# Kernel tuning notes

Hardware: AMD Instinct MI355X
Metric: run time of the kernel (lower is better)

## Reference

```python
import jax, jax.numpy as jnp
import numpy as np

N = 100000
E = 1600000
IN_C, HID_C, OUT_C = 64, 64, 40

def setup_inputs() -> dict:
    key = jax.random.key(0)
    ks = jax.random.split(key, 12)
    x = jax.random.normal(ks[0], (N, IN_C), dtype=jnp.float32)
    edge_index = jax.random.randint(ks[1], (2, E), 0, N, dtype=jnp.int32)
    def glorot(k, fan_in, fan_out):
        lim = float(np.sqrt(6.0 / (fan_in + fan_out)))
        return jax.random.uniform(k, (fan_in, fan_out), jnp.float32, -lim, lim)
    return {
        "x": x,
        "edge_index": edge_index,
        "W0_0": glorot(ks[2], IN_C, HID_C), "W1_0": glorot(ks[3], IN_C, HID_C), "b_0": jnp.zeros((HID_C,), jnp.float32),
        "W0_1": glorot(ks[4], HID_C, HID_C), "W1_1": glorot(ks[5], HID_C, HID_C), "b_1": jnp.zeros((HID_C,), jnp.float32),
        "W0_2": glorot(ks[6], HID_C, OUT_C), "W1_2": glorot(ks[7], HID_C, OUT_C), "b_2": jnp.zeros((OUT_C,), jnp.float32),
    }

def _cheb_norm(edge_index, num_nodes, dtype):
    # PyG ChebConv.__norm__ with normalization=None, edge_weight=None -> ones.
    # L = D - A; lambda_max = 2 * max(L weights); scaled: 2L/lambda_max - I.
    src, dst = edge_index[0], edge_index[1]
    w = jnp.ones((edge_index.shape[1],), dtype)
    deg = jax.ops.segment_sum(w, src, num_segments=num_nodes)
    lam = 2.0 * jnp.maximum(jnp.max(deg), jnp.max(-w))
    scale = 2.0 / lam
    norm_edge = -w * scale            # off-diagonal entries
    norm_loop = deg * scale - 1.0     # diagonal entries (self-loop mask subtracts 1)
    return norm_edge, norm_loop

def _spmm(x, src, dst, norm_edge, norm_loop, num_nodes):
    # y[i] = sum_{e: src->i} norm_e * x[src_e] + norm_loop[i] * x[i]
    msg = norm_edge[:, None] * x[src]
    return jax.ops.segment_sum(msg, dst, num_segments=num_nodes) + norm_loop[:, None] * x

def reference(x, edge_index, W0_0, W1_0, b_0, W0_1, W1_1, b_1, W0_2, W1_2, b_2):
    num_nodes = x.shape[0]
    src, dst = edge_index[0], edge_index[1]
    norm_edge, norm_loop = _cheb_norm(edge_index, num_nodes, x.dtype)

    def cheb(h, W0, W1, b):
        # K=2: out = T0(L) h W0 + T1(L) h W1 + b, T0 = I, T1 = scaled L
        Tx1 = _spmm(h, src, dst, norm_edge, norm_loop, num_nodes)
        return h @ W0 + Tx1 @ W1 + b

    h = jax.nn.relu(cheb(x, W0_0, W1_0, b_0))   # dropout is identity in eval mode
    h = jax.nn.relu(cheb(h, W0_1, W1_1, b_1))
    h = cheb(h, W0_2, W1_2, b_2)
    return jax.nn.log_softmax(h, axis=-1)
```

## Files before the change

kernel.cpp:

```cpp
#include <hip/hip_runtime.h>
#include <math.h>

#define N_NODES 100000
#define N_EDGES 1600000
#define OUTC 40
#define PAIRS40 20

#define NC 32
#define CHUNK (N_EDGES / NC)

#define RANGE_H 32768
#define NR_H 4
#define NPAD_H (NR_H * RANGE_H)

#define RANGE_F 16384
#define NR_F 7

#define FILLB (NC * NR_F)
#define NB32 (N_NODES / 32)
#define GEMB ((NB32 + 3) / 4)

#define SCAN_BLOCK 1024
#define SCAN_NBLK ((N_NODES + SCAN_BLOCK - 1) / SCAN_BLOCK)

typedef float vf2 __attribute__((ext_vector_type(2)));
typedef __fp16 f16x2 __attribute__((ext_vector_type(2)));

__device__ inline unsigned pack_bf16x2(float lo, float hi) {
    unsigned a = __float_as_uint(lo), b = __float_as_uint(hi);
    a = (a + 0x7fffu + ((a >> 16) & 1u)) >> 16;
    b = (b + 0x7fffu + ((b >> 16) & 1u)) & 0xffff0000u;
    return a | b;
}
__device__ inline float bf_lo(unsigned u) { return __uint_as_float(u << 16); }
__device__ inline float bf_hi(unsigned u) { return __uint_as_float(u & 0xffff0000u); }

__device__ inline unsigned pk16(float a, float b) {
    f16x2 h = __builtin_amdgcn_cvt_pkrtz(a, b);
    return __builtin_bit_cast(unsigned, h);
}
__device__ inline f16x2 uph(unsigned u) { return __builtin_bit_cast(f16x2, u); }

__device__ inline float fdot2(f16x2 a, f16x2 b, float c) {
#if __has_builtin(__builtin_amdgcn_fdot2)
    return __builtin_amdgcn_fdot2(a, b, c, false);
#else
    float d;
    asm volatile("v_dot2_f32_f16 %0, %1, %2, %3" : "=v"(d) : "v"(a), "v"(b), "v"(c));
    return d;
#endif
}

#define DOT2_KP4(hq, w0_, w1_, w2_, w3_, p)                                  \
    {                                                                        \
        f16x2 h0 = uph((hq).x), h1 = uph((hq).y), h2 = uph((hq).z), h3 = uph((hq).w); \
        a0x[p] = fdot2(h0, uph((w0_).x), a0x[p]);                            \
        a0y[p] = fdot2(h0, uph((w0_).y), a0y[p]);                            \
        a1x[p] = fdot2(h0, uph((w0_).z), a1x[p]);                            \
        a1y[p] = fdot2(h0, uph((w0_).w), a1y[p]);                            \
        a0x[p] = fdot2(h1, uph((w1_).x), a0x[p]);                            \
        a0y[p] = fdot2(h1, uph((w1_).y), a0y[p]);                            \
        a1x[p] = fdot2(h1, uph((w1_).z), a1x[p]);                            \
        a1y[p] = fdot2(h1, uph((w1_).w), a1y[p]);                            \
        a0x[p] = fdot2(h2, uph((w2_).x), a0x[p]);                            \
        a0y[p] = fdot2(h2, uph((w2_).y), a0y[p]);                            \
        a1x[p] = fdot2(h2, uph((w2_).z), a1x[p]);                            \
        a1y[p] = fdot2(h2, uph((w2_).w), a1y[p]);                            \
        a0x[p] = fdot2(h3, uph((w3_).x), a0x[p]);                            \
        a0y[p] = fdot2(h3, uph((w3_).y), a0y[p]);                            \
        a1x[p] = fdot2(h3, uph((w3_).z), a1x[p]);                            \
        a1y[p] = fdot2(h3, uph((w3_).w), a1y[p]);                            \
    }

__global__ __launch_bounds__(1024) void k_hist(const int* __restrict__ src,
                                               const int* __restrict__ dst,
                                               unsigned short* __restrict__ Hs,
                                               unsigned short* __restrict__ Hd) {
    __shared__ unsigned h32[RANGE_H / 2];
    int c = blockIdx.x, r = blockIdx.y;
    const int* a = blockIdx.z ? dst : src;
    unsigned short* H = blockIdx.z ? Hd : Hs;
    for (int k = threadIdx.x; k < RANGE_H / 2; k += 1024) h32[k] = 0;
    __syncthreads();
    int r0 = r * RANGE_H;
    int e0 = c * CHUNK, e1 = e0 + CHUNK;
    for (int e = e0 + threadIdx.x; e < e1; e += 1024) {
        unsigned d = (unsigned)(a[e] - r0);
        if (d < RANGE_H) atomicAdd(&h32[d >> 1], 1u << ((d & 1) * 16));
    }
    __syncthreads();
    for (int k = threadIdx.x; k < RANGE_H; k += 1024)
        H[c * NPAD_H + r0 + k] = (unsigned short)((h32[k >> 1] >> ((k & 1) * 16)) & 0xffffu);
}

__global__ __launch_bounds__(SCAN_BLOCK) void k_scan1(const unsigned short* __restrict__ Hs,
                                                      const unsigned short* __restrict__ Hd,
                                                      int* __restrict__ rowptr,
                                                      int* __restrict__ blocksum,
                                                      int* __restrict__ deg_src,
                                                      int* __restrict__ maxdeg) {
    __shared__ int buf[2][SCAN_BLOCK];
    int t = threadIdx.x;
    int i = blockIdx.x * SCAN_BLOCK + t;
    int vs = 0, vd = 0;
    if (i < N_NODES) {
        #pragma unroll
        for (int c = 0; c < NC; c++) { vs += Hs[c * NPAD_H + i]; vd += Hd[c * NPAD_H + i]; }
        deg_src[i] = vs;
    }
    int m = vs;
    for (int off = 32; off; off >>= 1) m = max(m, __shfl_down(m, off));
    if ((t & 63) == 0) atomicMax(maxdeg, m);
    int pd = (vd + 7) & ~7;
    int cur = 0;
    buf[0][t] = pd;
    __syncthreads();
    for (int off = 1; off < SCAN_BLOCK; off <<= 1) {
        int nv = buf[cur][t];
        if (t >= off) nv += buf[cur][t - off];
        buf[1 - cur][t] = nv;
        cur = 1 - cur;
        __syncthreads();
    }
    int incl = buf[cur][t];
    if (i < N_NODES) rowptr[i + 1] = incl;
    if (t == SCAN_BLOCK - 1) blocksum[blockIdx.x] = incl;
}

__global__ __launch_bounds__(SCAN_BLOCK) void k_finalize(const int* __restrict__ blocksum,
                                                         int* __restrict__ rowptr,
                                                         const unsigned short* __restrict__ Hd,
                                                         int* __restrict__ Bd,
                                                         int* __restrict__ csr_src) {
    __shared__ int soff;
    int t = threadIdx.x, blk = blockIdx.x;
    if (t == 0) {
        int r = 0;
        for (int j = 0; j < blk; j++) r += blocksum[j];
        soff = r;
        if (blk == 0) rowptr[0] = 0;
    }
    __syncthreads();
    int i = blk * SCAN_BLOCK + t;
    if (i >= N_NODES) return;
    int tmp[NC];
    int s = 0;
    #pragma unroll
    for (int c = 0; c < NC; c++) { tmp[c] = Hd[c * NPAD_H + i]; s += tmp[c]; }
    int rf = rowptr[i + 1] + soff;
    rowptr[i + 1] = rf;
    int pd = (s + 7) & ~7;
    int run = rf - pd;
    #pragma unroll
    for (int c = 0; c < NC; c++) { Bd[c * NPAD_H + i] = run; run += tmp[c]; }
    for (int k = run; k < rf; k++) csr_src[k] = N_NODES;
}

__global__ __launch_bounds__(1024) void k_fill_gemm(const int* __restrict__ src,
                                                    const int* __restrict__ dst,
                                                    const int* __restrict__ basepos,
                                                    int* __restrict__ csr_src,
                                                    const float* __restrict__ hf,
                                                    const float* __restrict__ W0,
                                                    const float* __restrict__ W1,
                                                    const float* __restrict__ b,
                                                    const int* __restrict__ deg_src,
                                                    const int* __restrict__ maxdeg,
                                                    unsigned* __restrict__ G0b,
                                                    unsigned short* __restrict__ G1f8) {
    __shared__ union {
        int pos[RANGE_F];
        struct { uint4 swu[32 * 32]; unsigned shu[4 * 1024]; } g;
    } sm;
    int t = threadIdx.x;
    if (blockIdx.x < FILLB) {
        int c = blockIdx.x & 31, r = blockIdx.x >> 5;
        int r0 = r * RANGE_F;
        for (int k = t; k < RANGE_F; k += 1024) sm.pos[k] = basepos[c * NPAD_H + r0 + k];
        __syncthreads();
        int e0 = c * CHUNK, e1 = e0 + CHUNK;
        for (int e = e0 + t; e < e1; e += 1024) {
            unsigned d = (unsigned)(dst[e] - r0);
            if (d < RANGE_F) {
                int s = src[e];
                int p = atomicAdd(&sm.pos[d], 1);
                csr_src[p] = s;
            }
        }
        return;
    }
    int gb = blockIdx.x - FILLB;
    int sub = t >> 8, tt = t & 255;
    int nb = gb * 4 + sub;
    bool ok = nb < NB32;
    const float2* W02 = (const float2*)W0;
    const float2* W12 = (const float2*)W1;
    {
        int kp = t >> 5, c2 = t & 31;
        float2 a  = W02[(kp * 2) * 32 + c2];
        float2 bb = W02[(kp * 2 + 1) * 32 + c2];
        float2 cc = W12[(kp * 2) * 32 + c2];
        float2 dd = W12[(kp * 2 + 1) * 32 + c2];
        sm.g.swu[t] = make_uint4(pk16(a.x, bb.x), pk16(a.y, bb.y), pk16(cc.x, dd.x), pk16(cc.y, dd.y));
    }
    if (ok) {
        const float4* h4 = (const float4*)(hf + (size_t)(nb * 32) * 64);
        float4 f0 = h4[tt * 2], f1 = h4[tt * 2 + 1];
        ((uint4*)(sm.g.shu + sub * 1024))[tt] =
            make_uint4(pk16(f0.x, f0.y), pk16(f0.z, f0.w), pk16(f1.x, f1.y), pk16(f1.z, f1.w));
    }
    if (blockIdx.x == FILLB && t < 16) ((unsigned*)G1f8)[N_NODES * 16 + t] = 0;
    __syncthreads();
    if (!ok) return;
    int c2 = tt & 31, rg = tt >> 5;
    int i0 = nb * 32;
    const unsigned* shu = sm.g.shu + sub * 1024;
    float scale = 1.0f / (float)(*maxdeg);
    float2 b2 = ((const float2*)b)[c2];
    float a0x[4], a0y[4], a1x[4], a1y[4];
    #pragma unroll
    for (int p = 0; p < 4; p++) { a0x[p] = b2.x; a0y[p] = b2.y; a1x[p] = 0.f; a1y[p] = 0.f; }
    #pragma unroll
    for (int kp4 = 0; kp4 < 32; kp4 += 4) {
        uint4 w0 = sm.g.swu[(kp4 + 0) * 32 + c2];
        uint4 w1 = sm.g.swu[(kp4 + 1) * 32 + c2];
        uint4 w2 = sm.g.swu[(kp4 + 2) * 32 + c2];
        uint4 w3 = sm.g.swu[(kp4 + 3) * 32 + c2];
        #pragma unroll
        for (int p = 0; p < 4; p++) {
            uint4 hq = ((const uint4*)(shu + (rg + 8 * p) * 32))[kp4 >> 2];
            DOT2_KP4(hq, w0, w1, w2, w3, p);
        }
    }
    #pragma unroll
    for (int p = 0; p < 4; p++) {
        int row = i0 + rg + 8 * p;
        float nl = (float)deg_src[row] * scale - 1.0f;
        G0b[row * 32 + c2] = pack_bf16x2(a0x[p] + nl * a1x[p], a0y[p] + nl * a1y[p]);
        int pk = __builtin_amdgcn_cvt_pk_fp8_f32(a1x[p], a1y[p], 0, false);
        G1f8[row * 32 + c2] = (unsigned short)(pk & 0xffff);
    }
}

__global__ __launch_bounds__(256, 8) void k_fs64_g64(const unsigned* __restrict__ G0b_in,
                                                     const unsigned char* __restrict__ g1_in,
                                                     const int* __restrict__ rowptr,
                                                     const int* __restrict__ csr_src,
                                                     const int* __restrict__ deg_src,
                                                     const int* __restrict__ maxdeg,
                                                     const float* __restrict__ W0,
                                                     const float* __restrict__ W1,
                                                     const float* __restrict__ b,
                                                     unsigned* __restrict__ G0b_out,
                                                     unsigned short* __restrict__ G1f8_out) {
    __shared__ uint4 swu[32 * 32];
    __shared__ unsigned shu[32 * 32];
    int t = threadIdx.x;
    const float2* W02 = (const float2*)W0;
    const float2* W12 = (const float2*)W1;
    for (int cell = t; cell < 1024; cell += 256) {
        int kp = cell >> 5, c2 = cell & 31;
        float2 a  = W02[(kp * 2) * 32 + c2];
        float2 bb = W02[(kp * 2 + 1) * 32 + c2];
        float2 cc = W12[(kp * 2) * 32 + c2];
        float2 dd = W12[(kp * 2 + 1) * 32 + c2];
        swu[cell] = make_uint4(pk16(a.x, bb.x), pk16(a.y, bb.y), pk16(cc.x, dd.x), pk16(cc.y, dd.y));
    }
    int waveId = t >> 6, lane = t & 63;
    int ch = lane & 7;
    int local = waveId * 8 + (lane >> 3);
    int node = blockIdx.x * 32 + local;
    float scale = 1.0f / (float)(*maxdeg);
    int e0 = rowptr[node], e1 = rowptr[node + 1];
    int octbase = lane & 56;
    vf2 acc[4];
    acc[0] = 0.f; acc[1] = 0.f; acc[2] = 0.f; acc[3] = 0.f;
    uint2 u[8];
    int idxB = 0;
    int e = e0;
    if (e < e1) {
        int idxA = csr_src[e + ch];
        if (e + 8 < e1) idxB = csr_src[e + 8 + ch];
        #pragma unroll
        for (int j = 0; j < 8; j++) {
            int s = __shfl(idxA, octbase | j);
            u[j] = ((const uint2*)(g1_in + (size_t)s * 64))[ch];
        }
    }
    while (e < e1) {
        int en = e + 8;
        int idxC = 0;
        if (en + 8 < e1) idxC = csr_src[en + 8 + ch];
        uint2 n[8];
        if (en < e1) {
            #pragma unroll
            for (int j = 0; j < 8; j++) {
                int s = __shfl(idxB, octbase | j);
                n[j] = ((const uint2*)(g1_in + (size_t)s * 64))[ch];
            }
        }
        #pragma unroll
        for (int j = 0; j < 8; j++) {
            acc[0] += __builtin_amdgcn_cvt_pk_f32_fp8((int)u[j].x, false);
            acc[1] += __builtin_amdgcn_cvt_pk_f32_fp8((int)u[j].x, true);
            acc[2] += __builtin_amdgcn_cvt_pk_f32_fp8((int)u[j].y, false);
            acc[3] += __builtin_amdgcn_cvt_pk_f32_fp8((int)u[j].y, true);
        }
        #pragma unroll
        for (int j = 0; j < 8; j++) u[j] = n[j];
        idxB = idxC;
        e = en;
    }
    uint4 g = ((const uint4*)(G0b_in + (size_t)node * 32))[ch];
    float v0 = fmaxf(bf_lo(g.x) - scale * acc[0].x, 0.f);
    float v1 = fmaxf(bf_hi(g.x) - scale * acc[0].y, 0.f);
    float v2 = fmaxf(bf_lo(g.y) - scale * acc[1].x, 0.f);
    float v3 = fmaxf(bf_hi(g.y) - scale * acc[1].y, 0.f);
    float v4 = fmaxf(bf_lo(g.z) - scale * acc[2].x, 0.f);
    float v5 = fmaxf(bf_hi(g.z) - scale * acc[2].y, 0.f);
    float v6 = fmaxf(bf_lo(g.w) - scale * acc[3].x, 0.f);
    float v7 = fmaxf(bf_hi(g.w) - scale * acc[3].y, 0.f);
    ((uint4*)shu)[local * 8 + ch] = make_uint4(pk16(v0, v1), pk16(v2, v3), pk16(v4, v5), pk16(v6, v7));
    if (blockIdx.x == 0 && t < 16) ((unsigned*)G1f8_out)[N_NODES * 16 + t] = 0;
    __syncthreads();
    int c2 = t & 31, rg = t >> 5;
    int i0 = blockIdx.x * 32;
    float2 b2 = ((const float2*)b)[c2];
    float a0x[4], a0y[4], a1x[4], a1y[4];
    #pragma unroll
    for (int p = 0; p < 4; p++) { a0x[p] = b2.x; a0y[p] = b2.y; a1x[p] = 0.f; a1y[p] = 0.f; }
    #pragma unroll
    for (int kp4 = 0; kp4 < 32; kp4 += 4) {
        uint4 w0 = swu[(kp4 + 0) * 32 + c2];
        uint4 w1 = swu[(kp4 + 1) * 32 + c2];
        uint4 w2 = swu[(kp4 + 2) * 32 + c2];
        uint4 w3 = swu[(kp4 + 3) * 32 + c2];
        #pragma unroll
        for (int p = 0; p < 4; p++) {
            uint4 hq = ((const uint4*)(shu + (rg + 8 * p) * 32))[kp4 >> 2];
            DOT2_KP4(hq, w0, w1, w2, w3, p);
        }
    }
    #pragma unroll
    for (int p = 0; p < 4; p++) {
        int row = i0 + rg + 8 * p;
        float nl = (float)deg_src[row] * scale - 1.0f;
        G0b_out[row * 32 + c2] = pack_bf16x2(a0x[p] + nl * a1x[p], a0y[p] + nl * a1y[p]);
        int pk = __builtin_amdgcn_cvt_pk_fp8_f32(a1x[p], a1y[p], 0, false);
        G1f8_out[row * 32 + c2] = (unsigned short)(pk & 0xffff);
    }
}

__global__ __launch_bounds__(256, 8) void k_fs64_g40(const unsigned* __restrict__ G0b_in,
                                                     const unsigned char* __restrict__ g1_in,
                                                     const int* __restrict__ rowptr,
                                                     const int* __restrict__ csr_src,
                                                     const int* __restrict__ deg_src,
                                                     const int* __restrict__ maxdeg,
                                                     const float* __restrict__ W0,
                                                     const float* __restrict__ W1,
                                                     const float* __restrict__ b,
                                                     unsigned* __restrict__ G0b_out,
                                                     unsigned short* __restrict__ G1f8_out) {
    __shared__ uint4 swu[32 * PAIRS40];
    __shared__ unsigned shu[32 * 32];
    int t = threadIdx.x;
    const float2* W02 = (const float2*)W0;
    const float2* W12 = (const float2*)W1;
    for (int cell = t; cell < 32 * PAIRS40; cell += 256) {
        int kp = cell / PAIRS40, c2 = cell % PAIRS40;
        float2 a  = W02[(kp * 2) * PAIRS40 + c2];
        float2 bb = W02[(kp * 2 + 1) * PAIRS40 + c2];
        float2 cc = W12[(kp * 2) * PAIRS40 + c2];
        float2 dd = W12[(kp * 2 + 1) * PAIRS40 + c2];
        swu[cell] = make_uint4(pk16(a.x, bb.x), pk16(a.y, bb.y), pk16(cc.x, dd.x), pk16(cc.y, dd.y));
    }
    int waveId = t >> 6, lane = t & 63;
    int ch = lane & 7;
    int local = waveId * 8 + (lane >> 3);
    int node = blockIdx.x * 32 + local;
    float scale = 1.0f / (float)(*maxdeg);
    int e0 = rowptr[node], e1 = rowptr[node + 1];
    int octbase = lane & 56;
    vf2 acc[4];
    acc[0] = 0.f; acc[1] = 0.f; acc[2] = 0.f; acc[3] = 0.f;
    uint2 u[8];
    int idxB = 0;
    int e = e0;
    if (e < e1) {
        int idxA = csr_src[e + ch];
        if (e + 8 < e1) idxB = csr_src[e + 8 + ch];
        #pragma unroll
        for (int j = 0; j < 8; j++) {
            int s = __shfl(idxA, octbase | j);
            u[j] = ((const uint2*)(g1_in + (size_t)s * 64))[ch];
        }
    }
    while (e < e1) {
        int en = e + 8;
        int idxC = 0;
        if (en + 8 < e1) idxC = csr_src[en + 8 + ch];
        uint2 n[8];
        if (en < e1) {
            #pragma unroll
            for (int j = 0; j < 8; j++) {
                int s = __shfl(idxB, octbase | j);
                n[j] = ((const uint2*)(g1_in + (size_t)s * 64))[ch];
            }
        }
        #pragma unroll
        for (int j = 0; j < 8; j++) {
            acc[0] += __builtin_amdgcn_cvt_pk_f32_fp8((int)u[j].x, false);
            acc[1] += __builtin_amdgcn_cvt_pk_f32_fp8((int)u[j].x, true);
            acc[2] += __builtin_amdgcn_cvt_pk_f32_fp8((int)u[j].y, false);
            acc[3] += __builtin_amdgcn_cvt_pk_f32_fp8((int)u[j].y, true);
        }
        #pragma unroll
        for (int j = 0; j < 8; j++) u[j] = n[j];
        idxB = idxC;
        e = en;
    }
    uint4 g = ((const uint4*)(G0b_in + (size_t)node * 32))[ch];
    float v0 = fmaxf(bf_lo(g.x) - scale * acc[0].x, 0.f);
    float v1 = fmaxf(bf_hi(g.x) - scale * acc[0].y, 0.f);
    float v2 = fmaxf(bf_lo(g.y) - scale * acc[1].x, 0.f);
    float v3 = fmaxf(bf_hi(g.y) - scale * acc[1].y, 0.f);
    float v4 = fmaxf(bf_lo(g.z) - scale * acc[2].x, 0.f);
    float v5 = fmaxf(bf_hi(g.z) - scale * acc[2].y, 0.f);
    float v6 = fmaxf(bf_lo(g.w) - scale * acc[3].x, 0.f);
    float v7 = fmaxf(bf_hi(g.w) - scale * acc[3].y, 0.f);
    ((uint4*)shu)[local * 8 + ch] = make_uint4(pk16(v0, v1), pk16(v2, v3), pk16(v4, v5), pk16(v6, v7));
    if (blockIdx.x == 0 && t < 10) ((unsigned*)G1f8_out)[N_NODES * 10 + t] = 0;
    __syncthreads();
    int c2 = t & 31, rg = t >> 5;
    if (c2 >= PAIRS40) return;
    int i0 = blockIdx.x * 32;
    float2 b2 = ((const float2*)b)[c2];
    float a0x[4], a0y[4], a1x[4], a1y[4];
    #pragma unroll
    for (int p = 0; p < 4; p++) { a0x[p] = b2.x; a0y[p] = b2.y; a1x[p] = 0.f; a1y[p] = 0.f; }
    #pragma unroll
    for (int kp4 = 0; kp4 < 32; kp4 += 4) {
        uint4 w0 = swu[(kp4 + 0) * PAIRS40 + c2];
        uint4 w1 = swu[(kp4 + 1) * PAIRS40 + c2];
        uint4 w2 = swu[(kp4 + 2) * PAIRS40 + c2];
        uint4 w3 = swu[(kp4 + 3) * PAIRS40 + c2];
        #pragma unroll
        for (int p = 0; p < 4; p++) {
            uint4 hq = ((const uint4*)(shu + (rg + 8 * p) * 32))[kp4 >> 2];
            DOT2_KP4(hq, w0, w1, w2, w3, p);
        }
    }
    #pragma unroll
    for (int p = 0; p < 4; p++) {
        int row = i0 + rg + 8 * p;
        float nl = (float)deg_src[row] * scale - 1.0f;
        G0b_out[row * PAIRS40 + c2] = pack_bf16x2(a0x[p] + nl * a1x[p], a0y[p] + nl * a1y[p]);
        int pk = __builtin_amdgcn_cvt_pk_fp8_f32(a1x[p], a1y[p], 0, false);
        G1f8_out[row * PAIRS40 + c2] = (unsigned short)(pk & 0xffff);
    }
}

__global__ __launch_bounds__(256, 8) void k_spmm40(const unsigned* __restrict__ G0b,
                                                   const unsigned char* __restrict__ g1,
                                                   const int* __restrict__ rowptr,
                                                   const int* __restrict__ csr_src,
                                                   const int* __restrict__ maxdeg,
                                                   float* __restrict__ out) {
    int t = threadIdx.x;
    int waveId = t >> 6, lane = t & 63;
    int ch = lane & 7;
    bool act = ch < 5;
    int node = blockIdx.x * 32 + waveId * 8 + (lane >> 3);
    float scale = 1.0f / (float)(*maxdeg);
    int e0 = rowptr[node], e1 = rowptr[node + 1];
    int octbase = lane & 56;
    vf2 acc[4];
    acc[0] = 0.f; acc[1] = 0.f; acc[2] = 0.f; acc[3] = 0.f;
    uint2 u[8];
    int idxB = 0;
    int e = e0;
    if (e < e1) {
        int idxA = csr_src[e + ch];
        if (e + 8 < e1) idxB = csr_src[e + 8 + ch];
        #pragma unroll
        for (int j = 0; j < 8; j++) {
            int s = __shfl(idxA, octbase | j);
            if (act) u[j] = ((const uint2*)(g1 + (size_t)s * 40))[ch];
        }
    }
    while (e < e1) {
        int en = e + 8;
        int idxC = 0;
        if (en + 8 < e1) idxC = csr_src[en + 8 + ch];
        uint2 n[8];
        if (en < e1) {
            #pragma unroll
            for (int j = 0; j < 8; j++) {
                int s = __shfl(idxB, octbase | j);
                if (act) n[j] = ((const uint2*)(g1 + (size_t)s * 40))[ch];
            }
        }
        if (act) {
            #pragma unroll
            for (int j = 0; j < 8; j++) {
                acc[0] += __builtin_amdgcn_cvt_pk_f32_fp8((int)u[j].x, false);
                acc[1] += __builtin_amdgcn_cvt_pk_f32_fp8((int)u[j].x, true);
                acc[2] += __builtin_amdgcn_cvt_pk_f32_fp8((int)u[j].y, false);
                acc[3] += __builtin_amdgcn_cvt_pk_f32_fp8((int)u[j].y, true);
            }
        }
        #pragma unroll
        for (int j = 0; j < 8; j++) u[j] = n[j];
        idxB = idxC;
        e = en;
    }
    float v[8];
    float m = -INFINITY;
    if (act) {
        uint4 g = ((const uint4*)(G0b + (size_t)node * PAIRS40))[ch];
        v[0] = bf_lo(g.x) - scale * acc[0].x;
        v[1] = bf_hi(g.x) - scale * acc[0].y;
        v[2] = bf_lo(g.y) - scale * acc[1].x;
        v[3] = bf_hi(g.y) - scale * acc[1].y;
        v[4] = bf_lo(g.z) - scale * acc[2].x;
        v[5] = bf_hi(g.z) - scale * acc[2].y;
        v[6] = bf_lo(g.w) - scale * acc[3].x;
        v[7] = bf_hi(g.w) - scale * acc[3].y;
        #pragma unroll
        for (int q = 0; q < 8; q++) m = fmaxf(m, v[q]);
    }
    m = fmaxf(m, __shfl_xor(m, 1));
    m = fmaxf(m, __shfl_xor(m, 2));
    m = fmaxf(m, __shfl_xor(m, 4));
    float s = 0.f;
    if (act) {
        #pragma unroll
        for (int q = 0; q < 8; q++) s += __expf(v[q] - m);
    }
    s += __shfl_xor(s, 1);
    s += __shfl_xor(s, 2);
    s += __shfl_xor(s, 4);
    float ls = __logf(s);
    if (act) {
        float4 oA, oB;
        oA.x = v[0] - m - ls; oA.y = v[1] - m - ls; oA.z = v[2] - m - ls; oA.w = v[3] - m - ls;
        oB.x = v[4] - m - ls; oB.y = v[5] - m - ls; oB.z = v[6] - m - ls; oB.w = v[7] - m - ls;
        float4* o4 = (float4*)(out + (size_t)node * 40);
        o4[ch * 2] = oA;
        o4[ch * 2 + 1] = oB;
    }
}


extern "C" void kernel_launch(void* const* d_in, const int* in_sizes, int n_in,
                              void* d_out, int out_size, void* d_ws, size_t ws_size,
                              hipStream_t stream) {
    const float* x   = (const float*)d_in[0];
    const int* ei    = (const int*)d_in[1];
    const int* src   = ei;
    const int* dst   = ei + N_EDGES;
    const float* W0_0 = (const float*)d_in[2];
    const float* W1_0 = (const float*)d_in[3];
    const float* b_0  = (const float*)d_in[4];
    const float* W0_1 = (const float*)d_in[5];
    const float* W1_1 = (const float*)d_in[6];
    const float* b_1  = (const float*)d_in[7];
    const float* W0_2 = (const float*)d_in[8];
    const float* W1_2 = (const float*)d_in[9];
    const float* b_2  = (const float*)d_in[10];
    float* outp = (float*)d_out;

    int* ip = (int*)d_ws;
    int* deg_src  = ip;
    int* rowptr   = ip + 100000;
    int* blocksum = ip + 200064;
    int* maxdeg   = ip + 200192;
    int* csr_src  = ip + 200256;
    unsigned short* Hs = (unsigned short*)(ip + 2700256);
    unsigned short* Hd = (unsigned short*)(ip + 4797408);
    int* Bd       = ip + 6894560;
    unsigned* GA0 = (unsigned*)(ip + 11088864);
    unsigned short* GA1 = (unsigned short*)(ip + 14288864);
    unsigned* GB0 = (unsigned*)(ip + 15888928);
    unsigned short* GB1 = (unsigned short*)(ip + 19088928);

    (void)hipMemsetAsync(maxdeg, 0, sizeof(int), stream);

    k_hist<<<dim3(NC, NR_H, 2), 1024, 0, stream>>>(src, dst, Hs, Hd);
    k_scan1<<<SCAN_NBLK, SCAN_BLOCK, 0, stream>>>(Hs, Hd, rowptr, blocksum, deg_src, maxdeg);
    k_finalize<<<SCAN_NBLK, SCAN_BLOCK, 0, stream>>>(blocksum, rowptr, Hd, Bd, csr_src);

    k_fill_gemm<<<FILLB + GEMB, 1024, 0, stream>>>(src, dst, Bd, csr_src,
                                                   x, W0_0, W1_0, b_0, deg_src, maxdeg, GA0, GA1);

    const int GS = N_NODES / 32;

    k_fs64_g64<<<GS, 256, 0, stream>>>(GA0, (const unsigned char*)GA1, rowptr, csr_src,
                                       deg_src, maxdeg, W0_1, W1_1, b_1, GB0, GB1);
    k_fs64_g40<<<GS, 256, 0, stream>>>(GB0, (const unsigned char*)GB1, rowptr, csr_src,
                                       deg_src, maxdeg, W0_2, W1_2, b_2, GA0, GA1);
    k_spmm40<<<GS, 256, 0, stream>>>(GA0, (const unsigned char*)GA1, rowptr, csr_src, maxdeg, outp);
}
```

Before: 296.9 us.

## Deepen gather prefetch to two edge batches in SpMM kernels and retune fill blocks

The three edge-gather SpMM kernels now keep two batches of neighbour rows in flight (double-lookahead software pipeline) instead of one, so more memory latency can be hidden per wave. Launch bounds drop from 8 to 6 waves per SIMD to make room for the extra registers. Separately, the CSR fill stage changes NR_F from 7 to 8 range blocks per chunk and remaps the block index so neighbouring blocks share an edge chunk. The risk is lower occupancy offsetting the gain from deeper prefetch.

```diff
diff --git a/kernel.cpp b/kernel.cpp
--- a/kernel.cpp
+++ b/kernel.cpp
@@ -14,7 +14,7 @@
 #define NPAD_H (NR_H * RANGE_H)
 
 #define RANGE_F 16384
-#define NR_F 7
+#define NR_F 8
 
 #define FILLB (NC * NR_F)
 #define NB32 (N_NODES / 32)
@@ -174,7 +174,7 @@
     } sm;
     int t = threadIdx.x;
     if (blockIdx.x < FILLB) {
-        int c = blockIdx.x & 31, r = blockIdx.x >> 5;
+        int c = blockIdx.x >> 3, r = blockIdx.x & 7;
         int r0 = r * RANGE_F;
         for (int k = t; k < RANGE_F; k += 1024) sm.pos[k] = basepos[c * NPAD_H + r0 + k];
         __syncthreads();
@@ -242,7 +242,7 @@
     }
 }
 
-__global__ __launch_bounds__(256, 8) void k_fs64_g64(const unsigned* __restrict__ G0b_in,
+__global__ __launch_bounds__(256, 6) void k_fs64_g64(const unsigned* __restrict__ G0b_in,
                                                      const unsigned char* __restrict__ g1_in,
                                                      const int* __restrict__ rowptr,
                                                      const int* __restrict__ csr_src,
@@ -275,28 +275,37 @@
     int octbase = lane & 56;
     vf2 acc[4];
     acc[0] = 0.f; acc[1] = 0.f; acc[2] = 0.f; acc[3] = 0.f;
-    uint2 u[8];
-    int idxB = 0;
+    uint2 u[8], n[8];
+    int idxC = 0;
     int e = e0;
     if (e < e1) {
         int idxA = csr_src[e + ch];
-        if (e + 8 < e1) idxB = csr_src[e + 8 + ch];
+        int idxB = 0;
+        if (e + 8 < e1)  idxB = csr_src[e + 8 + ch];
+        if (e + 16 < e1) idxC = csr_src[e + 16 + ch];
         #pragma unroll
         for (int j = 0; j < 8; j++) {
             int s = __shfl(idxA, octbase | j);
             u[j] = ((const uint2*)(g1_in + (size_t)s * 64))[ch];
         }
-    }
-    while (e < e1) {
-        int en = e + 8;
-        int idxC = 0;
-        if (en + 8 < e1) idxC = csr_src[en + 8 + ch];
-        uint2 n[8];
-        if (en < e1) {
+        if (e + 8 < e1) {
             #pragma unroll
             for (int j = 0; j < 8; j++) {
                 int s = __shfl(idxB, octbase | j);
                 n[j] = ((const uint2*)(g1_in + (size_t)s * 64))[ch];
+            }
+        }
+    }
+    while (e < e1) {
+        int en = e + 8;
+        int idxD = 0;
+        if (en + 16 < e1) idxD = csr_src[en + 16 + ch];
+        uint2 m[8];
+        if (en + 8 < e1) {
+            #pragma unroll
+            for (int j = 0; j < 8; j++) {
+                int s = __shfl(idxC, octbase | j);
+                m[j] = ((const uint2*)(g1_in + (size_t)s * 64))[ch];
             }
         }
         #pragma unroll
@@ -307,8 +316,8 @@
             acc[3] += __builtin_amdgcn_cvt_pk_f32_fp8((int)u[j].y, true);
         }
         #pragma unroll
-        for (int j = 0; j < 8; j++) u[j] = n[j];
-        idxB = idxC;
+        for (int j = 0; j < 8; j++) { u[j] = n[j]; n[j] = m[j]; }
+        idxC = idxD;
         e = en;
     }
     uint4 g = ((const uint4*)(G0b_in + (size_t)node * 32))[ch];
@@ -351,7 +360,7 @@
     }
 }
 
-__global__ __launch_bounds__(256, 8) void k_fs64_g40(const unsigned* __restrict__ G0b_in,
+__global__ __launch_bounds__(256, 6) void k_fs64_g40(const unsigned* __restrict__ G0b_in,
                                                      const unsigned char* __restrict__ g1_in,
                                                      const int* __restrict__ rowptr,
                                                      const int* __restrict__ csr_src,
@@ -384,28 +393,37 @@
     int octbase = lane & 56;
     vf2 acc[4];
     acc[0] = 0.f; acc[1] = 0.f; acc[2] = 0.f; acc[3] = 0.f;
-    uint2 u[8];
-    int idxB = 0;
+    uint2 u[8], n[8];
+    int idxC = 0;
     int e = e0;
     if (e < e1) {
         int idxA = csr_src[e + ch];
-        if (e + 8 < e1) idxB = csr_src[e + 8 + ch];
+        int idxB = 0;
+        if (e + 8 < e1)  idxB = csr_src[e + 8 + ch];
+        if (e + 16 < e1) idxC = csr_src[e + 16 + ch];
         #pragma unroll
         for (int j = 0; j < 8; j++) {
             int s = __shfl(idxA, octbase | j);
             u[j] = ((const uint2*)(g1_in + (size_t)s * 64))[ch];
         }
-    }
-    while (e < e1) {
-        int en = e + 8;
-        int idxC = 0;
-        if (en + 8 < e1) idxC = csr_src[en + 8 + ch];
-        uint2 n[8];
-        if (en < e1) {
+        if (e + 8 < e1) {
             #pragma unroll
             for (int j = 0; j < 8; j++) {
                 int s = __shfl(idxB, octbase | j);
                 n[j] = ((const uint2*)(g1_in + (size_t)s * 64))[ch];
+            }
+        }
+    }
+    while (e < e1) {
+        int en = e + 8;
+        int idxD = 0;
+        if (en + 16 < e1) idxD = csr_src[en + 16 + ch];
+        uint2 m[8];
+        if (en + 8 < e1) {
+            #pragma unroll
+            for (int j = 0; j < 8; j++) {
+                int s = __shfl(idxC, octbase | j);
+                m[j] = ((const uint2*)(g1_in + (size_t)s * 64))[ch];
             }
         }
         #pragma unroll
@@ -416,8 +434,8 @@
             acc[3] += __builtin_amdgcn_cvt_pk_f32_fp8((int)u[j].y, true);
         }
         #pragma unroll
-        for (int j = 0; j < 8; j++) u[j] = n[j];
-        idxB = idxC;
+        for (int j = 0; j < 8; j++) { u[j] = n[j]; n[j] = m[j]; }
+        idxC = idxD;
         e = en;
     }
     uint4 g = ((const uint4*)(G0b_in + (size_t)node * 32))[ch];
@@ -461,7 +479,7 @@
     }
 }
 
-__global__ __launch_bounds__(256, 8) void k_spmm40(const unsigned* __restrict__ G0b,
+__global__ __launch_bounds__(256, 6) void k_spmm40(const unsigned* __restrict__ G0b,
                                                    const unsigned char* __restrict__ g1,
                                                    const int* __restrict__ rowptr,
                                                    const int* __restrict__ csr_src,
@@ -477,28 +495,37 @@
     int octbase = lane & 56;
     vf2 acc[4];
     acc[0] = 0.f; acc[1] = 0.f; acc[2] = 0.f; acc[3] = 0.f;
-    uint2 u[8];
-    int idxB = 0;
+    uint2 u[8], n[8];
+    int idxC = 0;
     int e = e0;
     if (e < e1) {
         int idxA = csr_src[e + ch];
-        if (e + 8 < e1) idxB = csr_src[e + 8 + ch];
+        int idxB = 0;
+        if (e + 8 < e1)  idxB = csr_src[e + 8 + ch];
+        if (e + 16 < e1) idxC = csr_src[e + 16 + ch];
         #pragma unroll
         for (int j = 0; j < 8; j++) {
             int s = __shfl(idxA, octbase | j);
             if (act) u[j] = ((const uint2*)(g1 + (size_t)s * 40))[ch];
         }
-    }
-    while (e < e1) {
-        int en = e + 8;
-        int idxC = 0;
-        if (en + 8 < e1) idxC = csr_src[en + 8 + ch];
-        uint2 n[8];
-        if (en < e1) {
+        if (e + 8 < e1) {
             #pragma unroll
             for (int j = 0; j < 8; j++) {
                 int s = __shfl(idxB, octbase | j);
                 if (act) n[j] = ((const uint2*)(g1 + (size_t)s * 40))[ch];
+            }
+        }
+    }
+    while (e < e1) {
+        int en = e + 8;
+        int idxD = 0;
+        if (en + 16 < e1) idxD = csr_src[en + 16 + ch];
+        uint2 m[8];
+        if (en + 8 < e1) {
+            #pragma unroll
+            for (int j = 0; j < 8; j++) {
+                int s = __shfl(idxC, octbase | j);
+                if (act) m[j] = ((const uint2*)(g1 + (size_t)s * 40))[ch];
             }
         }
         if (act) {
@@ -511,8 +538,8 @@
             }
         }
         #pragma unroll
-        for (int j = 0; j < 8; j++) u[j] = n[j];
-        idxB = idxC;
+        for (int j = 0; j < 8; j++) { u[j] = n[j]; n[j] = m[j]; }
+        idxC = idxD;
         e = en;
     }
     float v[8];
```

Result: no change. 298.1 us (+0.4%).
